# Performance work log

Measured on AMD Instinct MI355X. Metric: run time of the kernel, lower is better.

Reference implementation:

```python
import jax, jax.numpy as jnp
import numpy as np

NC = 80            # num_classes
REG_MAX = 16
STRIDES = (8, 16, 32)
IMG = 640.0
TOPK = 10
TAL_ALPHA = 0.5
TAL_BETA = 6.0
L_BOX, L_CLS, L_DFL = 7.5, 0.5, 1.5
EPS = 1e-9
NEG = -1e8


def bbox_iou(b1, b2, ciou=False, eps=1e-7):
    # b1, b2: (..., 4) xyxy, broadcastable
    inter_wh = jnp.clip(jnp.minimum(b1[..., 2:], b2[..., 2:]) - jnp.maximum(b1[..., :2], b2[..., :2]), 0.0)
    inter = inter_wh[..., 0] * inter_wh[..., 1]
    w1 = jnp.clip(b1[..., 2] - b1[..., 0], 0.0); h1 = jnp.clip(b1[..., 3] - b1[..., 1], 0.0)
    w2 = jnp.clip(b2[..., 2] - b2[..., 0], 0.0); h2 = jnp.clip(b2[..., 3] - b2[..., 1], 0.0)
    union = w1 * h1 + w2 * h2 - inter + eps
    iou = inter / union
    if not ciou:
        return iou
    cx1 = (b1[..., 0] + b1[..., 2]) * 0.5; cy1 = (b1[..., 1] + b1[..., 3]) * 0.5
    cx2 = (b2[..., 0] + b2[..., 2]) * 0.5; cy2 = (b2[..., 1] + b2[..., 3]) * 0.5
    rho2 = (cx2 - cx1) ** 2 + (cy2 - cy1) ** 2
    cw = jnp.maximum(b1[..., 2], b2[..., 2]) - jnp.minimum(b1[..., 0], b2[..., 0])
    ch = jnp.maximum(b1[..., 3], b2[..., 3]) - jnp.minimum(b1[..., 1], b2[..., 1])
    c2 = cw ** 2 + ch ** 2 + eps
    v = (4.0 / np.pi ** 2) * (jnp.arctan(w2 / (h2 + eps)) - jnp.arctan(w1 / (h1 + eps))) ** 2
    alpha = jax.lax.stop_gradient(v / (1.0 - iou + v + eps))  # torch computes alpha under no_grad
    return iou - (rho2 / c2 + alpha * v)


def _assign_one(pred_scores, pred_bboxes, anchor_points, gt_labels, gt_bboxes):
    """TaskAlignedAssigner for one image.
    pred_scores (N,nc), pred_bboxes (N,4), anchor_points (N,2), gt_labels (M,), gt_bboxes (M,4).
    Returns target_bboxes (N,4), target_scores (N,nc), fg_mask (N,)."""
    N = pred_bboxes.shape[0]; M = gt_bboxes.shape[0]
    gl = jnp.clip(gt_labels.astype(jnp.int32), 0, NC - 1)
    x = anchor_points[:, 0]; y = anchor_points[:, 1]
    l = x[:, None] - gt_bboxes[None, :, 0]
    t = y[:, None] - gt_bboxes[None, :, 1]
    r = gt_bboxes[None, :, 2] - x[:, None]
    b = gt_bboxes[None, :, 3] - y[:, None]
    in_gts = (l > 0) & (t > 0) & (r > 0) & (b > 0)                     # (N,M)
    ious = bbox_iou(pred_bboxes[:, None, :], gt_bboxes[None, :, :])    # (N,M)
    cls_score = pred_scores[:, gl]                                     # (N,M)
    align = jnp.clip(cls_score, 0.0) ** TAL_ALPHA * jnp.clip(ious, 0.0) ** TAL_BETA
    align = jnp.where(in_gts, align, NEG)
    k = min(TOPK, N)
    _, topk_idx = jax.lax.top_k(align.T, k)                            # (M,k) indices into N
    mask_topk = jnp.zeros((M, N), dtype=bool).at[jnp.arange(M)[:, None], topk_idx].set(True).T
    mask_pos = mask_topk & in_gts                                      # (N,M)
    ious_pos = jnp.where(mask_pos, ious, -1.0)
    max_iou = ious_pos.max(axis=1)
    gt_idx = ious_pos.argmax(axis=1)                                   # (N,)
    fg_mask = max_iou > -0.5
    metric_pos = jnp.where(mask_pos, align, NEG)
    metric_max = jnp.clip(metric_pos.max(axis=0), EPS)                 # (M,)
    rows = jnp.arange(N)
    score = align[rows, gt_idx] / metric_max[gt_idx] * ious[rows, gt_idx]
    score = jnp.clip(score, 0.0, 1.0) * fg_mask.astype(pred_scores.dtype)
    tcls = gl[gt_idx]
    target_scores = jnp.zeros((N, NC), dtype=pred_scores.dtype).at[rows, tcls].set(score)
    target_bboxes = jnp.where(fg_mask[:, None], gt_bboxes[gt_idx], 0.0)
    return target_bboxes, target_scores, fg_mask


def _df_loss(reg_logits, target):
    # reg_logits (B,N,4,R) logits, target (B,N,4) float in [0,R-1] -> (B,N)
    t = jnp.clip(target, 0.0, float(REG_MAX - 1))
    left = jnp.floor(t).astype(jnp.int32)
    right = jnp.minimum(left + 1, REG_MAX - 1)
    wl = right.astype(t.dtype) - t
    wr = t - left.astype(t.dtype)
    same = right == left
    wl = jnp.where(same, 1.0, wl)
    wr = jnp.where(same, 0.0, wr)
    logp = jax.nn.log_softmax(reg_logits, axis=-1)
    ll = -jnp.take_along_axis(logp, left[..., None], axis=-1)[..., 0]
    lr = -jnp.take_along_axis(logp, right[..., None], axis=-1)[..., 0]
    return (ll * wl + lr * wr).sum(axis=-1)


def _forward(p0, p1, p2, gt_bboxes, gt_labels):
    preds = [p0, p1, p2]
    B = p0.shape[0]
    reg_ch = 4 * REG_MAX
    cls_list, reg_list, ap_list, st_list = [], [], [], []
    for p, s in zip(preds, STRIDES):
        _, _, h, w = p.shape
        reg = p[:, :reg_ch]
        cls = p[:, reg_ch:]
        cls_list.append(cls.transpose(0, 2, 3, 1).reshape(B, -1, NC))
        reg_list.append(reg.transpose(0, 2, 3, 1).reshape(B, -1, 4, REG_MAX))
        gy, gx = jnp.meshgrid(jnp.arange(h), jnp.arange(w), indexing='ij')
        pts = jnp.stack([(gx + 0.5) * s, (gy + 0.5) * s], axis=-1).reshape(-1, 2).astype(p.dtype)
        ap_list.append(pts)
        st_list.append(jnp.full((h * w,), float(s), dtype=p.dtype))
    cls_logits = jnp.concatenate(cls_list, axis=1)      # (B,N,nc)
    reg_logits = jnp.concatenate(reg_list, axis=1)      # (B,N,4,R)
    anchor_points = jnp.concatenate(ap_list, axis=0)    # (N,2)
    stride_t = jnp.concatenate(st_list, axis=0)         # (N,)
    pred_scores = jax.nn.sigmoid(cls_logits)
    proj = jnp.arange(REG_MAX, dtype=cls_logits.dtype)
    dist = (jax.nn.softmax(reg_logits, axis=-1) * proj).sum(-1) * stride_t[None, :, None]  # (B,N,4)
    ax = anchor_points[:, 0]; ay = anchor_points[:, 1]
    pred_bboxes = jnp.stack([ax - dist[..., 0], ay - dist[..., 1], ax + dist[..., 2], ay + dist[..., 3]], axis=-1)
    # --- TAL assignment (runs under no_grad in torch) ---
    tb, ts, fg = jax.vmap(lambda ps, pb, gl, gb: _assign_one(ps, pb, anchor_points, gl, gb))(
        jax.lax.stop_gradient(pred_scores), jax.lax.stop_gradient(pred_bboxes), gt_labels, gt_bboxes)
    tb = jax.lax.stop_gradient(tb)
    ts = jax.lax.stop_gradient(ts)
    ts_sum = jnp.maximum(ts.sum(), 1.0)
    # --- cls: BCE with logits over all anchors/classes ---
    z = cls_logits
    bce = jnp.clip(z, 0.0) - z * ts + jnp.log1p(jnp.exp(-jnp.abs(z)))
    loss_cls = bce.sum() / ts_sum
    # --- box: CIoU weighted by target score, fg only ---
    weight = ts.sum(-1) * fg.astype(ts.dtype)           # (B,N)
    ciou = bbox_iou(pred_bboxes, tb, ciou=True)         # (B,N)
    loss_box = ((1.0 - ciou) * weight).sum() / ts_sum
    # --- dfl ---
    inv_s = 1.0 / stride_t
    tl = (ax - tb[..., 0]) * inv_s
    tt = (ay - tb[..., 1]) * inv_s
    tr = (tb[..., 2] - ax) * inv_s
    tbm = (tb[..., 3] - ay) * inv_s
    target_ltrb = jnp.clip(jnp.stack([tl, tt, tr, tbm], axis=-1), 0.0, float(REG_MAX - 1))
    dfl = _df_loss(reg_logits, target_ltrb)             # (B,N)
    loss_dfl = (dfl * weight).sum() / ts_sum
    return L_BOX * loss_box + L_CLS * loss_cls + L_DFL * loss_dfl


def setup_inputs() -> dict:
    key = jax.random.key(0)
    k0, k1, k2, kc, kw, kl = jax.random.split(key, 6)
    B, C = 16, 4 * REG_MAX + NC
    p0 = jax.random.normal(k0, (B, C, 80, 80), dtype=jnp.float32)
    p1 = jax.random.normal(k1, (B, C, 40, 40), dtype=jnp.float32)
    p2 = jax.random.normal(k2, (B, C, 20, 20), dtype=jnp.float32)
    M = 32
    cxy = jax.random.uniform(kc, (B, M, 2), minval=64.0, maxval=IMG - 64.0)
    wh = jax.random.uniform(kw, (B, M, 2), minval=16.0, maxval=128.0)
    gt_bboxes = jnp.concatenate([cxy - wh * 0.5, cxy + wh * 0.5], axis=-1).astype(jnp.float32)
    gt_labels = jax.random.randint(kl, (B, M), 0, NC, dtype=jnp.int32).astype(jnp.int64)
    return {"p0": p0, "p1": p1, "p2": p2, "gt_bboxes": gt_bboxes, "gt_labels": gt_labels}


def reference(p0, p1, p2, gt_bboxes, gt_labels):
    return _forward(p0, p1, p2, gt_bboxes, gt_labels)
```

## Files before the change

kernel.cpp:

```cpp
#include <hip/hip_runtime.h>

#define BATCH 16
#define NANCH 8400
#define MGT 32
#define NCLS 80
#define RCH 64
#define NCH 144
#define TOPKK 10
#define MAXC 576
#define TKB 512
#define BCEB 2625
#define TOTB (TKB + BCEB)
#define FINB 525

struct AInfo { int lvl, pos, W, HW; float s, ax, ay; };

__device__ __forceinline__ AInfo anchor_of(int n) {
  AInfo a;
  if (n < 6400)      { a.lvl = 0; a.pos = n;        a.W = 80; a.HW = 6400; a.s = 8.f;  }
  else if (n < 8000) { a.lvl = 1; a.pos = n - 6400; a.W = 40; a.HW = 1600; a.s = 16.f; }
  else               { a.lvl = 2; a.pos = n - 8000; a.W = 20; a.HW = 400;  a.s = 32.f; }
  int px = a.pos % a.W, py = a.pos / a.W;
  a.ax = (px + 0.5f) * a.s;
  a.ay = (py + 0.5f) * a.s;
  return a;
}

__device__ __forceinline__ const float* lvl_ptr(const float* p0, const float* p1,
                                                const float* p2, int lvl) {
  return lvl == 0 ? p0 : (lvl == 1 ? p1 : p2);
}

__device__ __forceinline__ float4 decode_box(const float* __restrict__ p, size_t chbase,
                                             int HW, float s, float ax, float ay) {
  float d[4];
  #pragma unroll
  for (int q = 0; q < 4; ++q) {
    float z[16]; float zm = -1e30f;
    #pragma unroll
    for (int j = 0; j < 16; ++j) {
      z[j] = p[chbase + (size_t)(q * 16 + j) * HW];
      zm = fmaxf(zm, z[j]);
    }
    float se = 0.f, ae = 0.f;
    #pragma unroll
    for (int j = 0; j < 16; ++j) {
      float e = __expf(z[j] - zm);
      se += e; ae += e * (float)j;
    }
    d[q] = ae / se * s;
  }
  return make_float4(ax - d[0], ay - d[1], ax + d[2], ay + d[3]);
}

__device__ __forceinline__ float iou_xyxy(float4 a, float4 b) {
  float ix = fmaxf(fminf(a.z, b.z) - fmaxf(a.x, b.x), 0.f);
  float iy = fmaxf(fminf(a.w, b.w) - fmaxf(a.y, b.y), 0.f);
  float inter = ix * iy;
  float w1 = fmaxf(a.z - a.x, 0.f), h1 = fmaxf(a.w - a.y, 0.f);
  float w2 = fmaxf(b.z - b.x, 0.f), h2 = fmaxf(b.w - b.y, 0.f);
  float uni = w1 * h1 + w2 * h2 - inter + 1e-7f;
  return inter / uni;
}

__device__ __forceinline__ float ciou_xyxy(float4 a, float4 b) {
  const float eps = 1e-7f;
  float ix = fmaxf(fminf(a.z, b.z) - fmaxf(a.x, b.x), 0.f);
  float iy = fmaxf(fminf(a.w, b.w) - fmaxf(a.y, b.y), 0.f);
  float inter = ix * iy;
  float w1 = fmaxf(a.z - a.x, 0.f), h1 = fmaxf(a.w - a.y, 0.f);
  float w2 = fmaxf(b.z - b.x, 0.f), h2 = fmaxf(b.w - b.y, 0.f);
  float uni = w1 * h1 + w2 * h2 - inter + eps;
  float iou = inter / uni;
  float cx1 = (a.x + a.z) * 0.5f, cy1 = (a.y + a.w) * 0.5f;
  float cx2 = (b.x + b.z) * 0.5f, cy2 = (b.y + b.w) * 0.5f;
  float rho2 = (cx2 - cx1) * (cx2 - cx1) + (cy2 - cy1) * (cy2 - cy1);
  float cw = fmaxf(a.z, b.z) - fminf(a.x, b.x);
  float ch = fmaxf(a.w, b.w) - fminf(a.y, b.y);
  float c2 = cw * cw + ch * ch + eps;
  const float kpi = 4.f / (float)(M_PI * M_PI);
  float dat = atanf(w2 / (h2 + eps)) - atanf(w1 / (h1 + eps));
  float v = kpi * dat * dat;
  float alpha = v / (1.f - iou + v + eps);
  return iou - (rho2 / c2 + alpha * v);
}

__device__ __forceinline__ float block_sum256(float v) {
  __shared__ float sm[4];
  #pragma unroll
  for (int off = 32; off; off >>= 1) v += __shfl_xor(v, off);
  __syncthreads();
  if ((threadIdx.x & 63) == 0) sm[threadIdx.x >> 6] = v;
  __syncthreads();
  return (threadIdx.x == 0) ? (sm[0] + sm[1] + sm[2] + sm[3]) : 0.f;
}

__device__ __forceinline__ double block_sum256d(double v) {
  __shared__ double smd[4];
  #pragma unroll
  for (int off = 32; off; off >>= 1) v += __shfl_xor(v, off);
  __syncthreads();
  if ((threadIdx.x & 63) == 0) smd[threadIdx.x >> 6] = v;
  __syncthreads();
  return (threadIdx.x == 0) ? (smd[0] + smd[1] + smd[2] + smd[3]) : 0.0;
}

__global__ __launch_bounds__(256) void k_one(
    const float* __restrict__ p0, const float* __restrict__ p1, const float* __restrict__ p2,
    const float* __restrict__ gtb, const int* __restrict__ gtl,
    float* __restrict__ metric_max, unsigned long long* __restrict__ slots,
    float* __restrict__ bce_part) {
  __shared__ float val[MAXC];
  __shared__ int   idx[MAXC];
  __shared__ float cio[MAXC];
  __shared__ float rv[4];
  __shared__ int   ri[4], rs[4], sdone[1];
  int blk = blockIdx.x, tid = threadIdx.x;

  if (blk >= TKB) {
    int r = blk - TKB;
    int i = r * 256 + tid;
    float lb = 0.f;
    #pragma unroll
    for (int j = 0; j < 4; ++j) {
      int u = i + j * 672000;
      int b = u / 168000;
      int rr = u % 168000;
      const float4* src;
      if (rr < 128000)      src = (const float4*)p0 + ((size_t)(b * NCH + RCH) * 1600 + rr);
      else if (rr < 160000) src = (const float4*)p1 + ((size_t)(b * NCH + RCH) * 400 + (rr - 128000));
      else                  src = (const float4*)p2 + ((size_t)(b * NCH + RCH) * 100 + (rr - 160000));
      float4 z4 = *src;
      lb += fmaxf(z4.x, 0.f) + __logf(1.f + __expf(-fabsf(z4.x)));
      lb += fmaxf(z4.y, 0.f) + __logf(1.f + __expf(-fabsf(z4.y)));
      lb += fmaxf(z4.z, 0.f) + __logf(1.f + __expf(-fabsf(z4.z)));
      lb += fmaxf(z4.w, 0.f) + __logf(1.f + __expf(-fabsf(z4.w)));
    }
    float tot = block_sum256(lb);
    if (tid == 0) bce_part[r] = tot;
    return;
  }

  int b = blk >> 5, m = blk & 31;
  float4 g = ((const float4*)gtb)[b * MGT + m];
  int gl = min(max(gtl[b * MGT + m], 0), NCLS - 1);

  const int   Ws[3] = {80, 40, 20};
  const float ss[3] = {8.f, 16.f, 32.f};
  const int   nb[3] = {0, 6400, 8000};
  int x0[3], y0[3], nxl[3], cb[3];
  int cnt = 0;
  #pragma unroll
  for (int L = 0; L < 3; ++L) {
    float s = ss[L]; int W = Ws[L];
    int ax0 = max((int)floorf(g.x / s - 0.5f), 0);
    int ax1 = min((int)ceilf (g.z / s - 0.5f), W - 1);
    int ay0 = max((int)floorf(g.y / s - 0.5f), 0);
    int ay1 = min((int)ceilf (g.w / s - 0.5f), W - 1);
    int nx = max(ax1 - ax0 + 1, 0);
    int ny = max(ay1 - ay0 + 1, 0);
    x0[L] = ax0; y0[L] = ay0; nxl[L] = nx;
    cb[L] = cnt; cnt += nx * ny;
  }
  int C = min(cnt, MAXC);

  for (int t = tid; t < C; t += 256) {
    int L = (t >= cb[2]) ? 2 : (t >= cb[1]) ? 1 : 0;
    int r = t - cb[L];
    int ix = r % nxl[L], iy = r / nxl[L];
    int px = x0[L] + ix, py = y0[L] + iy;
    float ax = (px + 0.5f) * ss[L], ay = (py + 0.5f) * ss[L];
    float al = -3e38f, iou = 0.f; int n = 0x7fffffff;
    if (ax > g.x && ay > g.y && ax < g.z && ay < g.w) {
      int W = Ws[L];
      int HW = (L == 0) ? 6400 : (L == 1) ? 1600 : 400;
      int pos = py * W + px;
      n = nb[L] + pos;
      const float* p = lvl_ptr(p0, p1, p2, L);
      size_t chbase = (size_t)b * NCH * HW + pos;
      float4 pb = decode_box(p, chbase, HW, ss[L], ax, ay);
      iou = iou_xyxy(pb, g);
      float z = p[chbase + (size_t)(RCH + gl) * HW];
      float sg = 1.f / (1.f + __expf(-z));
      float i3 = iou * iou * iou;
      al = sqrtf(sg) * i3 * i3;
    }
    val[t] = al; idx[t] = n; cio[t] = iou;
  }
  __syncthreads();

  float mmax = -1.f;
  for (int k = 0; k < TOPKK; ++k) {
    float bv = -3e38f; int bn = 0x7fffffff, bs = 0;
    for (int t = tid; t < C; t += 256) {
      float v = val[t]; int n2 = idx[t];
      if (v > bv || (v == bv && n2 < bn)) { bv = v; bn = n2; bs = t; }
    }
    #pragma unroll
    for (int off = 32; off; off >>= 1) {
      float ov = __shfl_xor(bv, off);
      int   on = __shfl_xor(bn, off);
      int   os = __shfl_xor(bs, off);
      if (ov > bv || (ov == bv && on < bn)) { bv = ov; bn = on; bs = os; }
    }
    if ((tid & 63) == 0) { rv[tid >> 6] = bv; ri[tid >> 6] = bn; rs[tid >> 6] = bs; }
    __syncthreads();
    if (tid == 0) {
      #pragma unroll
      for (int w = 1; w < 4; ++w)
        if (rv[w] > bv || (rv[w] == bv && ri[w] < bn)) { bv = rv[w]; bn = ri[w]; bs = rs[w]; }
      if (bv >= 0.f) {
        mmax = fmaxf(mmax, bv);
        unsigned long long key = (1ULL << 62) |
                                 ((unsigned long long)__float_as_uint(cio[bs]) << 6) |
                                 (unsigned long long)(31 - m);
        atomicMax(&slots[(size_t)b * NANCH + bn], key);
        val[bs] = -3e38f;
        sdone[0] = 0;
      } else sdone[0] = 1;
    }
    __syncthreads();
    if (sdone[0]) break;
  }
  if (tid == 0) metric_max[b * MGT + m] = fmaxf(mmax, 1e-9f);
}

__global__ __launch_bounds__(256) void k_fin(
    const float* __restrict__ p0, const float* __restrict__ p1, const float* __restrict__ p2,
    const float* __restrict__ gtb, const int* __restrict__ gtl,
    const float* __restrict__ metric_max, const unsigned long long* __restrict__ slots,
    float4* __restrict__ fin_part) {
  int i = blockIdx.x * 256 + threadIdx.x;
  unsigned long long key = slots[i];
  float ts_p = 0.f, zc_p = 0.f, box_p = 0.f, dfl_p = 0.f;
  if (key) {
    int b = i / NANCH, n = i % NANCH;
    int m = 31 - (int)(key & 63ULL);
    float iou = __uint_as_float((unsigned int)((key >> 6) & 0xFFFFFFFFULL));
    AInfo A = anchor_of(n);
    float4 g = ((const float4*)gtb)[b * MGT + m];
    int gl = min(max(gtl[b * MGT + m], 0), NCLS - 1);
    const float* p = lvl_ptr(p0, p1, p2, A.lvl);
    size_t base = (size_t)b * NCH * A.HW + A.pos;

    float z = p[base + (size_t)(RCH + gl) * A.HW];
    float sg = 1.f / (1.f + __expf(-z));
    float i3 = iou * iou * iou;
    float align = sqrtf(sg) * i3 * i3;
    float mm = metric_max[b * MGT + m];
    float score = fminf(fmaxf(align / mm * iou, 0.f), 1.f);

    ts_p = score;
    zc_p = z * score;

    float inv_s = 1.f / A.s;
    float targ0 = (A.ax - g.x) * inv_s;
    float targ1 = (A.ay - g.y) * inv_s;
    float targ2 = (g.z - A.ax) * inv_s;
    float targ3 = (g.w - A.ay) * inv_s;

    float d[4]; float dfl = 0.f;
    #pragma unroll
    for (int sd = 0; sd < 4; ++sd) {
      float tg = sd == 0 ? targ0 : sd == 1 ? targ1 : sd == 2 ? targ2 : targ3;
      float t = fminf(fmaxf(tg, 0.f), 15.f);
      int left = (int)floorf(t);
      int right = min(left + 1, 15);
      float wl, wr;
      if (right == left) { wl = 1.f; wr = 0.f; }
      else               { wl = (float)right - t; wr = t - (float)left; }
      float zz[16]; float zm = -1e30f;
      #pragma unroll
      for (int j = 0; j < 16; ++j) {
        zz[j] = p[base + (size_t)(sd * 16 + j) * A.HW];
        zm = fmaxf(zm, zz[j]);
      }
      float se = 0.f, ae = 0.f, zl = 0.f, zr = 0.f;
      #pragma unroll
      for (int j = 0; j < 16; ++j) {
        float e = __expf(zz[j] - zm);
        se += e; ae += e * (float)j;
        if (j == left)  zl = zz[j];
        if (j == right) zr = zz[j];
      }
      d[sd] = ae / se * A.s;
      float logZ = zm + __logf(se);
      dfl += wl * (logZ - zl) + wr * (logZ - zr);
    }
    dfl_p = dfl * score;

    float4 pb = make_float4(A.ax - d[0], A.ay - d[1], A.ax + d[2], A.ay + d[3]);
    float ciou = ciou_xyxy(pb, g);
    box_p = (1.f - ciou) * score;
  }
  float s0 = block_sum256(box_p);
  float s1 = block_sum256(zc_p);
  float s2 = block_sum256(dfl_p);
  float s3 = block_sum256(ts_p);
  if (threadIdx.x == 0) fin_part[blockIdx.x] = make_float4(s0, s1, s2, s3);
}

__global__ void k_out(const float* __restrict__ bce_part, const float4* __restrict__ fin_part,
                      float* __restrict__ out) {
  int tid = threadIdx.x;
  double sb = 0.0, s0 = 0.0, s1 = 0.0, s2 = 0.0, s3 = 0.0;
  for (int t = tid; t < BCEB; t += 256) sb += (double)bce_part[t];
  for (int t = tid; t < FINB; t += 256) {
    float4 f = fin_part[t];
    s0 += (double)f.x; s1 += (double)f.y; s2 += (double)f.z; s3 += (double)f.w;
  }
  sb = block_sum256d(sb);
  s0 = block_sum256d(s0);
  s1 = block_sum256d(s1);
  s2 = block_sum256d(s2);
  s3 = block_sum256d(s3);
  if (tid == 0) {
    double ts = fmax(s3, 1.0);
    out[0] = (float)(7.5 * s0 / ts + 0.5 * (sb - s1) / ts + 1.5 * s2 / ts);
  }
}

extern "C" void kernel_launch(void* const* d_in, const int* in_sizes, int n_in,
                              void* d_out, int out_size, void* d_ws, size_t ws_size,
                              hipStream_t stream) {
  const float* p0  = (const float*)d_in[0];
  const float* p1  = (const float*)d_in[1];
  const float* p2  = (const float*)d_in[2];
  const float* gtb = (const float*)d_in[3];
  const int*   gtl = (const int*)d_in[4];
  float* out = (float*)d_out;

  char* ws = (char*)d_ws;
  float*  metric_max = (float*)ws;
  float*  bce_part   = (float*)(ws + 2048);
  float4* fin_part   = (float4*)(ws + 12560);
  unsigned long long* slots = (unsigned long long*)(ws + 20960);

  hipMemsetAsync(slots, 0, (size_t)BATCH * NANCH * 8, stream);
  k_one<<<TOTB, 256, 0, stream>>>(p0, p1, p2, gtb, gtl, metric_max, slots, bce_part);
  k_fin<<<FINB, 256, 0, stream>>>(p0, p1, p2, gtb, gtl, metric_max, slots, fin_part);
  k_out<<<1, 256, 0, stream>>>(bce_part, fin_part, out);
}
```

Before: 137.3 us.

## Drive final loss pass from compact per-GT top-k candidate list

The assignment kernel now also writes each GT's selected top-k anchors and IoUs into a compact list, padding unused entries with a sentinel. The final kernel walks this list of 5120 entries (20 blocks) instead of scanning all 134400 anchor slots (525 blocks). A candidate is kept only if it still owns the anchor slot after the atomicMax resolution, which avoids double counting. This cuts the dense slot read and the mostly-idle block launches, at the cost of an extra list write and a slot lookup per entry.

```diff
diff --git a/kernel.cpp b/kernel.cpp
--- a/kernel.cpp
+++ b/kernel.cpp
@@ -11,7 +11,9 @@
 #define TKB 512
 #define BCEB 2625
 #define TOTB (TKB + BCEB)
-#define FINB 525
+#define NLIST (BATCH * MGT * TOPKK)
+#define FINB (NLIST / 256)
+#define SENT (~0ULL)
 
 struct AInfo { int lvl, pos, W, HW; float s, ax, ay; };
 
@@ -109,7 +111,7 @@
     const float* __restrict__ p0, const float* __restrict__ p1, const float* __restrict__ p2,
     const float* __restrict__ gtb, const int* __restrict__ gtl,
     float* __restrict__ metric_max, unsigned long long* __restrict__ slots,
-    float* __restrict__ bce_part) {
+    unsigned long long* __restrict__ list, float* __restrict__ bce_part) {
   __shared__ float val[MAXC];
   __shared__ int   idx[MAXC];
   __shared__ float cio[MAXC];
@@ -144,6 +146,7 @@
   int b = blk >> 5, m = blk & 31;
   float4 g = ((const float4*)gtb)[b * MGT + m];
   int gl = min(max(gtl[b * MGT + m], 0), NCLS - 1);
+  unsigned long long* lst = list + (size_t)(b * MGT + m) * TOPKK;
 
   const int   Ws[3] = {80, 40, 20};
   const float ss[3] = {8.f, 16.f, 32.f};
@@ -190,7 +193,8 @@
   __syncthreads();
 
   float mmax = -1.f;
-  for (int k = 0; k < TOPKK; ++k) {
+  int k;
+  for (k = 0; k < TOPKK; ++k) {
     float bv = -3e38f; int bn = 0x7fffffff, bs = 0;
     for (int t = tid; t < C; t += 256) {
       float v = val[t]; int n2 = idx[t];
@@ -211,10 +215,12 @@
         if (rv[w] > bv || (rv[w] == bv && ri[w] < bn)) { bv = rv[w]; bn = ri[w]; bs = rs[w]; }
       if (bv >= 0.f) {
         mmax = fmaxf(mmax, bv);
+        unsigned int ib = __float_as_uint(cio[bs]);
         unsigned long long key = (1ULL << 62) |
-                                 ((unsigned long long)__float_as_uint(cio[bs]) << 6) |
+                                 ((unsigned long long)ib << 6) |
                                  (unsigned long long)(31 - m);
         atomicMax(&slots[(size_t)b * NANCH + bn], key);
+        lst[k] = ((unsigned long long)ib << 32) | (unsigned int)bn;
         val[bs] = -3e38f;
         sdone[0] = 0;
       } else sdone[0] = 1;
@@ -222,76 +228,86 @@
     __syncthreads();
     if (sdone[0]) break;
   }
-  if (tid == 0) metric_max[b * MGT + m] = fmaxf(mmax, 1e-9f);
+  if (tid == 0) {
+    for (int kk = k; kk < TOPKK; ++kk) lst[kk] = SENT;
+    metric_max[b * MGT + m] = fmaxf(mmax, 1e-9f);
+  }
 }
 
 __global__ __launch_bounds__(256) void k_fin(
     const float* __restrict__ p0, const float* __restrict__ p1, const float* __restrict__ p2,
     const float* __restrict__ gtb, const int* __restrict__ gtl,
     const float* __restrict__ metric_max, const unsigned long long* __restrict__ slots,
-    float4* __restrict__ fin_part) {
-  int i = blockIdx.x * 256 + threadIdx.x;
-  unsigned long long key = slots[i];
+    const unsigned long long* __restrict__ list, float4* __restrict__ fin_part) {
+  int e = blockIdx.x * 256 + threadIdx.x;
+  unsigned long long ent = list[e];
   float ts_p = 0.f, zc_p = 0.f, box_p = 0.f, dfl_p = 0.f;
-  if (key) {
-    int b = i / NANCH, n = i % NANCH;
-    int m = 31 - (int)(key & 63ULL);
-    float iou = __uint_as_float((unsigned int)((key >> 6) & 0xFFFFFFFFULL));
-    AInfo A = anchor_of(n);
-    float4 g = ((const float4*)gtb)[b * MGT + m];
-    int gl = min(max(gtl[b * MGT + m], 0), NCLS - 1);
-    const float* p = lvl_ptr(p0, p1, p2, A.lvl);
-    size_t base = (size_t)b * NCH * A.HW + A.pos;
-
-    float z = p[base + (size_t)(RCH + gl) * A.HW];
-    float sg = 1.f / (1.f + __expf(-z));
-    float i3 = iou * iou * iou;
-    float align = sqrtf(sg) * i3 * i3;
-    float mm = metric_max[b * MGT + m];
-    float score = fminf(fmaxf(align / mm * iou, 0.f), 1.f);
-
-    ts_p = score;
-    zc_p = z * score;
-
-    float inv_s = 1.f / A.s;
-    float targ0 = (A.ax - g.x) * inv_s;
-    float targ1 = (A.ay - g.y) * inv_s;
-    float targ2 = (g.z - A.ax) * inv_s;
-    float targ3 = (g.w - A.ay) * inv_s;
-
-    float d[4]; float dfl = 0.f;
-    #pragma unroll
-    for (int sd = 0; sd < 4; ++sd) {
-      float tg = sd == 0 ? targ0 : sd == 1 ? targ1 : sd == 2 ? targ2 : targ3;
-      float t = fminf(fmaxf(tg, 0.f), 15.f);
-      int left = (int)floorf(t);
-      int right = min(left + 1, 15);
-      float wl, wr;
-      if (right == left) { wl = 1.f; wr = 0.f; }
-      else               { wl = (float)right - t; wr = t - (float)left; }
-      float zz[16]; float zm = -1e30f;
+  if (ent != SENT) {
+    int b = e / (MGT * TOPKK);
+    int m = (e % (MGT * TOPKK)) / TOPKK;
+    int n = (int)(ent & 0xFFFFFFFFULL);
+    unsigned int ib = (unsigned int)(ent >> 32);
+    unsigned long long key = (1ULL << 62) |
+                             ((unsigned long long)ib << 6) |
+                             (unsigned long long)(31 - m);
+    if (slots[(size_t)b * NANCH + n] == key) {
+      float iou = __uint_as_float(ib);
+      AInfo A = anchor_of(n);
+      float4 g = ((const float4*)gtb)[b * MGT + m];
+      int gl = min(max(gtl[b * MGT + m], 0), NCLS - 1);
+      const float* p = lvl_ptr(p0, p1, p2, A.lvl);
+      size_t base = (size_t)b * NCH * A.HW + A.pos;
+
+      float z = p[base + (size_t)(RCH + gl) * A.HW];
+      float sg = 1.f / (1.f + __expf(-z));
+      float i3 = iou * iou * iou;
+      float align = sqrtf(sg) * i3 * i3;
+      float mm = metric_max[b * MGT + m];
+      float score = fminf(fmaxf(align / mm * iou, 0.f), 1.f);
+
+      ts_p = score;
+      zc_p = z * score;
+
+      float inv_s = 1.f / A.s;
+      float targ0 = (A.ax - g.x) * inv_s;
+      float targ1 = (A.ay - g.y) * inv_s;
+      float targ2 = (g.z - A.ax) * inv_s;
+      float targ3 = (g.w - A.ay) * inv_s;
+
+      float d[4]; float dfl = 0.f;
       #pragma unroll
-      for (int j = 0; j < 16; ++j) {
-        zz[j] = p[base + (size_t)(sd * 16 + j) * A.HW];
-        zm = fmaxf(zm, zz[j]);
+      for (int sd = 0; sd < 4; ++sd) {
+        float tg = sd == 0 ? targ0 : sd == 1 ? targ1 : sd == 2 ? targ2 : targ3;
+        float t = fminf(fmaxf(tg, 0.f), 15.f);
+        int left = (int)floorf(t);
+        int right = min(left + 1, 15);
+        float wl, wr;
+        if (right == left) { wl = 1.f; wr = 0.f; }
+        else               { wl = (float)right - t; wr = t - (float)left; }
+        float zz[16]; float zm = -1e30f;
+        #pragma unroll
+        for (int j = 0; j < 16; ++j) {
+          zz[j] = p[base + (size_t)(sd * 16 + j) * A.HW];
+          zm = fmaxf(zm, zz[j]);
+        }
+        float se = 0.f, ae = 0.f, zl = 0.f, zr = 0.f;
+        #pragma unroll
+        for (int j = 0; j < 16; ++j) {
+          float ex = __expf(zz[j] - zm);
+          se += ex; ae += ex * (float)j;
+          if (j == left)  zl = zz[j];
+          if (j == right) zr = zz[j];
+        }
+        d[sd] = ae / se * A.s;
+        float logZ = zm + __logf(se);
+        dfl += wl * (logZ - zl) + wr * (logZ - zr);
       }
-      float se = 0.f, ae = 0.f, zl = 0.f, zr = 0.f;
-      #pragma unroll
-      for (int j = 0; j < 16; ++j) {
-        float e = __expf(zz[j] - zm);
-        se += e; ae += e * (float)j;
-        if (j == left)  zl = zz[j];
-        if (j == right) zr = zz[j];
-      }
-      d[sd] = ae / se * A.s;
-      float logZ = zm + __logf(se);
-      dfl += wl * (logZ - zl) + wr * (logZ - zr);
-    }
-    dfl_p = dfl * score;
-
-    float4 pb = make_float4(A.ax - d[0], A.ay - d[1], A.ax + d[2], A.ay + d[3]);
-    float ciou = ciou_xyxy(pb, g);
-    box_p = (1.f - ciou) * score;
+      dfl_p = dfl * score;
+
+      float4 pb = make_float4(A.ax - d[0], A.ay - d[1], A.ax + d[2], A.ay + d[3]);
+      float ciou = ciou_xyxy(pb, g);
+      box_p = (1.f - ciou) * score;
+    }
   }
   float s0 = block_sum256(box_p);
   float s1 = block_sum256(zc_p);
@@ -334,10 +350,11 @@
   float*  metric_max = (float*)ws;
   float*  bce_part   = (float*)(ws + 2048);
   float4* fin_part   = (float4*)(ws + 12560);
-  unsigned long long* slots = (unsigned long long*)(ws + 20960);
+  unsigned long long* list  = (unsigned long long*)(ws + 12896);
+  unsigned long long* slots = (unsigned long long*)(ws + 53856);
 
   hipMemsetAsync(slots, 0, (size_t)BATCH * NANCH * 8, stream);
-  k_one<<<TOTB, 256, 0, stream>>>(p0, p1, p2, gtb, gtl, metric_max, slots, bce_part);
-  k_fin<<<FINB, 256, 0, stream>>>(p0, p1, p2, gtb, gtl, metric_max, slots, fin_part);
+  k_one<<<TOTB, 256, 0, stream>>>(p0, p1, p2, gtb, gtl, metric_max, slots, list, bce_part);
+  k_fin<<<FINB, 256, 0, stream>>>(p0, p1, p2, gtb, gtl, metric_max, slots, list, fin_part);
   k_out<<<1, 256, 0, stream>>>(bce_part, fin_part, out);
 }
```

New measurement: 143.7 us. 1.05x slower.
